# Performance work log

Measured on AMD Instinct MI355X. Metric: run time of the kernel, lower is better.

Reference implementation:

```python
import jax, jax.numpy as jnp
import numpy as np

B, L, D_MODEL, N_HEADS = 2, 2048, 1024, 16
D_HEAD = D_MODEL // N_HEADS
EPS = 1e-5


def setup_inputs() -> dict:
    key = jax.random.key(0)
    ks = jax.random.split(key, 10)
    x = jax.random.normal(ks[0], (B, L, D_MODEL), dtype=jnp.float32)
    # causal boolean mask [B, L, L]
    attn_mask = jnp.broadcast_to(jnp.tril(jnp.ones((L, L), dtype=bool)), (B, L, L))
    ts = jax.random.randint(ks[1], (B, L), 0, 10000)
    rope_lambda = jax.random.uniform(ks[2], (B, L, 1), dtype=jnp.float32)
    q_gate = jax.random.uniform(ks[3], (B, L, N_HEADS), dtype=jnp.float32)
    k_gate = jax.random.uniform(ks[4], (B, L, N_HEADS), dtype=jnp.float32)
    v_gate = jax.random.uniform(ks[5], (B, L, N_HEADS), dtype=jnp.float32)
    type_pair_bias = jax.random.normal(ks[6], (B, 1, L, L), dtype=jnp.float32)
    # parameters (torch Linear convention: y = x @ W.T + b)
    proj_w = jax.random.normal(ks[7], (4 * D_MODEL, D_MODEL), dtype=jnp.float32) * 0.02
    proj_b = jnp.zeros((4 * D_MODEL,), dtype=jnp.float32)
    out_w = jax.random.normal(ks[8], (D_MODEL, D_MODEL), dtype=jnp.float32) * 0.02
    out_b = jnp.zeros((D_MODEL,), dtype=jnp.float32)
    head_scale = jnp.ones((N_HEADS,), dtype=jnp.float32) * (D_HEAD ** -0.5)
    ln_gamma = jnp.ones((D_MODEL,), dtype=jnp.float32)
    ln_beta = jnp.zeros((D_MODEL,), dtype=jnp.float32)
    return {"x": x, "attn_mask": attn_mask, "ts": ts, "rope_lambda": rope_lambda,
            "q_gate": q_gate, "k_gate": k_gate, "v_gate": v_gate,
            "type_pair_bias": type_pair_bias, "proj_w": proj_w, "proj_b": proj_b,
            "out_w": out_w, "out_b": out_b, "head_scale": head_scale,
            "ln_gamma": ln_gamma, "ln_beta": ln_beta}


def _split_heads(t):
    b, l, _ = t.shape
    return t.reshape(b, l, N_HEADS, D_HEAD).transpose(0, 2, 1, 3)  # [B,H,L,Dh]


def _apply_rope(q, k, rope_lambda):
    # behavior-module RoPE: positions from cumsum of rope_lambda
    pos = jnp.cumsum(rope_lambda[..., 0], axis=1)  # [B, L]
    inv_freq = 1.0 / (10000.0 ** (jnp.arange(0, D_HEAD, 2, dtype=jnp.float32) / D_HEAD))
    freqs = pos[:, None, :, None] * inv_freq[None, None, None, :]  # [B,1,L,Dh/2]
    cos, sin = jnp.cos(freqs), jnp.sin(freqs)

    def rot(t):
        te, to = t[..., 0::2], t[..., 1::2]
        return jnp.concatenate([te * cos - to * sin, te * sin + to * cos], axis=-1)

    return rot(q), rot(k)


def reference(x, attn_mask, ts, rope_lambda, q_gate, k_gate, v_gate,
              type_pair_bias, proj_w, proj_b, out_w, out_b, head_scale,
              ln_gamma, ln_beta):
    b, l, d = x.shape
    h = jax.nn.silu(x @ proj_w.T + proj_b)  # [B,L,4D]
    u, v, q, k = jnp.split(h, 4, axis=-1)
    u, v, q, k = _split_heads(u), _split_heads(v), _split_heads(q), _split_heads(k)
    q, k = _apply_rope(q, k, rope_lambda)
    # multiplicative per-head gates: [B,L,H] -> [B,H,L,1]
    q = q * q_gate.transpose(0, 2, 1)[..., None]
    k = k * k_gate.transpose(0, 2, 1)[..., None]
    v = v * v_gate.transpose(0, 2, 1)[..., None]
    logits = jnp.einsum('bhid,bhjd->bhij', q, k)
    logits = logits * head_scale[None, :, None, None]
    # original does two adds: + type_pair_bias and + 3.0 * type_pair_bias
    logits = logits + type_pair_bias
    logits = logits + 3.0 * type_pair_bias
    logits = jax.nn.silu(logits)  # non-softmax SiLU attention
    logits = jnp.where(attn_mask[:, None, :, :], logits, 0.0)
    y = jnp.einsum('bhij,bhjd->bhid', logits, v)  # [B,H,L,Dh]
    y = y.transpose(0, 2, 1, 3).reshape(b, l, d)
    y = y * u.transpose(0, 2, 1, 3).reshape(b, l, d)  # gated output
    y = y @ out_w.T + out_b
    r = x + y  # dropout is identity in eval mode
    mu = jnp.mean(r, axis=-1, keepdims=True)
    var = jnp.mean((r - mu) ** 2, axis=-1, keepdims=True)
    return (r - mu) / jnp.sqrt(var + EPS) * ln_gamma + ln_beta
```

## Files before the change

### kernel.cpp

```cpp
#include <hip/hip_runtime.h>
#include <cstdint>
#include <cstddef>

typedef unsigned short u16;
typedef __attribute__((ext_vector_type(8))) short short8v;
typedef __attribute__((ext_vector_type(4))) float f32x4;

#define B_   2
#define L_   2048
#define D_   1024
#define NH_  16
#define DH_  64
#define M_   (B_*L_)
#define N4_  (4*D_)

__device__ __forceinline__ float bf2f(u16 u) {
  union { float f; unsigned int i; } v; v.i = ((unsigned int)u) << 16; return v.f;
}
__device__ __forceinline__ u16 f2bf(float f) {
  union { float f; unsigned int i; } v; v.f = f;
  unsigned int x = v.i;
  return (u16)((x + 0x7fffu + ((x >> 16) & 1u)) >> 16);
}
__device__ __forceinline__ unsigned int pk_bf16(float a, float b) {
#if __has_builtin(__builtin_amdgcn_cvt_pk_bf16_f32)
  auto r = __builtin_amdgcn_cvt_pk_bf16_f32(a, b);
  union { decltype(r) v; unsigned int u; } c; c.v = r; return c.u;
#else
  return (unsigned int)f2bf(a) | ((unsigned int)f2bf(b) << 16);
#endif
}
__device__ __forceinline__ float siluf(float x) { return x / (1.0f + __expf(-x)); }

__device__ __forceinline__ void gl2lds16(const u16* g, u16* l) {
  __builtin_amdgcn_global_load_lds(
      (const __attribute__((address_space(1))) unsigned int*)(const void*)g,
      (__attribute__((address_space(3))) unsigned int*)(void*)l,
      16, 0, 0);
}

__global__ __launch_bounds__(256) void k_conv_cum(const float* __restrict__ x,
                                                  const float* __restrict__ pw,
                                                  const float* __restrict__ ow,
                                                  const float* __restrict__ lam,
                                                  u16* __restrict__ xb,
                                                  u16* __restrict__ pwb,
                                                  u16* __restrict__ owb,
                                                  float* __restrict__ pos) {
  const int NX = M_ * D_ / 4, NP = N4_ * D_ / 4;
  int bid = blockIdx.x;
  int tid = threadIdx.x;
  if (bid < 9216) {
    int i = bid * 256 + tid;
    const float* src; u16* dst; int j;
    if (i < NX)            { src = x;  dst = xb;  j = i; }
    else if (i < NX + NP)  { src = pw; dst = pwb; j = i - NX; }
    else                   { src = ow; dst = owb; j = i - NX - NP; }
    float4 v = ((const float4*)src)[j];
    ushort4 o; o.x = f2bf(v.x); o.y = f2bf(v.y); o.z = f2bf(v.z); o.w = f2bf(v.w);
    ((ushort4*)dst)[j] = o;
  } else {
    int b = bid - 9216;
    const float* in = lam + (size_t)b * L_;
    float* out = pos + (size_t)b * L_;
    float loc[8], s = 0.0f;
#pragma unroll
    for (int i = 0; i < 8; ++i) { loc[i] = in[tid * 8 + i]; s += loc[i]; }
    __shared__ float sb[256];
    sb[tid] = s;
    __syncthreads();
    for (int off = 1; off < 256; off <<= 1) {
      float t = (tid >= off) ? sb[tid - off] : 0.0f;
      __syncthreads();
      sb[tid] += t;
      __syncthreads();
    }
    float run = sb[tid] - s;
#pragma unroll
    for (int i = 0; i < 8; ++i) { run += loc[i]; out[tid * 8 + i] = run; }
  }
}

__global__ __launch_bounds__(256, 4) void k_gemm1(const u16* __restrict__ A,
                                                  const u16* __restrict__ Bw,
                                                  const float* __restrict__ bias,
                                                  u16* __restrict__ hu, u16* __restrict__ hv,
                                                  u16* __restrict__ hq, u16* __restrict__ hk) {
  const int K = D_;
  int bn = blockIdx.x, bm = blockIdx.y, tid = threadIdx.x;
  int w = tid >> 6, lane = tid & 63, quad = lane >> 4, r16 = lane & 15;
  __shared__ __align__(16) u16 As[8192], Bs[8192];
  const u16* gA = A  + (size_t)(bm * 128) * K;
  const u16* gB = Bw + (size_t)(bn * 128) * K;
  int srow = tid >> 2, sc = tid & 3;
#pragma unroll
  for (int s = 0; s < 2; ++s) {
    int row = s * 64 + srow;
    int q = (sc - (row >> 1)) & 3;
    gl2lds16(gA + (size_t)row * K + q * 8, As + s * 2048 + w * 512);
    gl2lds16(gB + (size_t)row * K + q * 8, Bs + s * 2048 + w * 512);
  }
  f32x4 acc[4][4] = {};
  int wm = w & 1, wn = w >> 1;
  const int rowb = wm * 64, colb = wn * 64;
  for (int n = 0; n < 32; ++n) {
    __syncthreads();
    if (n + 1 < 32) {
      int kt = (n + 1) * 32, pb = (n + 1) & 1;
#pragma unroll
      for (int s = 0; s < 2; ++s) {
        int row = s * 64 + srow;
        int q = (sc - (row >> 1)) & 3;
        gl2lds16(gA + (size_t)row * K + kt + q * 8, As + pb * 4096 + s * 2048 + w * 512);
        gl2lds16(gB + (size_t)row * K + kt + q * 8, Bs + pb * 4096 + s * 2048 + w * 512);
      }
    }
    const u16* Ab = As + (n & 1) * 4096;
    const u16* Bb = Bs + (n & 1) * 4096;
    short8v af[4], bf[4];
#pragma unroll
    for (int mi = 0; mi < 4; ++mi) {
      int row = rowb + mi * 16 + r16;
      af[mi] = *(const short8v*)(Ab + (row * 4 + ((quad + (row >> 1)) & 3)) * 8);
    }
#pragma unroll
    for (int ni = 0; ni < 4; ++ni) {
      int row = colb + ni * 16 + r16;
      bf[ni] = *(const short8v*)(Bb + (row * 4 + ((quad + (row >> 1)) & 3)) * 8);
    }
#pragma unroll
    for (int mi = 0; mi < 4; ++mi)
#pragma unroll
      for (int ni = 0; ni < 4; ++ni)
        acc[mi][ni] = __builtin_amdgcn_mfma_f32_16x16x32_bf16(af[mi], bf[ni], acc[mi][ni], 0, 0, 0);
  }
  int nb = (bn * 128) >> 10;
  u16* dst = (nb == 0) ? hu : (nb == 1) ? hv : (nb == 2) ? hq : hk;
  int cbase = (bn * 128) & 1023;
  int row0 = bm * 128 + rowb;
#pragma unroll
  for (int ni = 0; ni < 4; ++ni) {
    int gcol = bn * 128 + colb + ni * 16 + r16;
    int lcol = cbase + colb + ni * 16 + r16;
    float bb = bias[gcol];
#pragma unroll
    for (int mi = 0; mi < 4; ++mi)
#pragma unroll
      for (int r = 0; r < 4; ++r) {
        int row = row0 + mi * 16 + quad * 4 + r;
        dst[(size_t)row * D_ + lcol] = f2bf(siluf(acc[mi][ni][r] + bb));
      }
  }
}

__global__ __launch_bounds__(256) void k_rope_vt(const u16* __restrict__ hq, const u16* __restrict__ hk,
                                                 const u16* __restrict__ hv,
                                                 const float* __restrict__ pos,
                                                 const float* __restrict__ qg, const float* __restrict__ kg,
                                                 const float* __restrict__ vg,
                                                 const float* __restrict__ hsc,
                                                 u16* __restrict__ Qb, u16* __restrict__ Kb,
                                                 u16* __restrict__ Vtb) {
  int bid = blockIdx.x;
  int tid = threadIdx.x;
  if (bid < 2048) {
    int idx = bid * 256 + tid;
    int j4 = idx & 7;
    int l  = (idx >> 3) & 2047;
    int bh = idx >> 14;
    int b = bh >> 4, hh = bh & 15;
    int row = b * L_ + l;
    float p = pos[row];
    float qs = qg[(size_t)row * NH_ + hh] * hsc[hh];
    float kgv = kg[(size_t)row * NH_ + hh];
    const u16* hqr = hq + (size_t)row * D_ + hh * DH_ + j4 * 8;
    const u16* hkr = hk + (size_t)row * D_ + hh * DH_ + j4 * 8;
    short8v qv = *(const short8v*)hqr;
    short8v kv = *(const short8v*)hkr;
    size_t ob = ((size_t)bh * L_ + l) * DH_ + j4 * 4;
    u16 qeo[4], qoo[4], keo[4], koo[4];
#pragma unroll
    for (int t = 0; t < 4; ++t) {
      int j = j4 * 4 + t;
      float inv = __expf(-(float)j * 0.28782313662425574f);
      float a = p * inv;
      float c, s;
      __sincosf(a, &s, &c);
      float qe = bf2f((u16)qv[2 * t]), qo = bf2f((u16)qv[2 * t + 1]);
      float ke = bf2f((u16)kv[2 * t]), ko = bf2f((u16)kv[2 * t + 1]);
      qeo[t] = f2bf((qe * c - qo * s) * qs);
      qoo[t] = f2bf((qe * s + qo * c) * qs);
      keo[t] = f2bf((ke * c - ko * s) * kgv);
      koo[t] = f2bf((ke * s + ko * c) * kgv);
    }
    *(ushort4*)(Qb + ob)      = make_ushort4(qeo[0], qeo[1], qeo[2], qeo[3]);
    *(ushort4*)(Qb + ob + 32) = make_ushort4(qoo[0], qoo[1], qoo[2], qoo[3]);
    *(ushort4*)(Kb + ob)      = make_ushort4(keo[0], keo[1], keo[2], keo[3]);
    *(ushort4*)(Kb + ob + 32) = make_ushort4(koo[0], koo[1], koo[2], koo[3]);
  } else {
    int b2 = bid - 2048;
    int lt = b2 & 31;
    int bh = b2 >> 5;
    int b = bh >> 4, hh = bh & 15;
    __shared__ u16 t[64][68];
    {
      int r = tid >> 2, cg = tid & 3;
      int row = b * L_ + lt * 64 + r;
      float gv = vg[(size_t)row * NH_ + hh];
      const u16* src = hv + (size_t)row * D_ + hh * DH_ + cg * 16;
      short8v v0 = ((const short8v*)src)[0];
      short8v v1 = ((const short8v*)src)[1];
#pragma unroll
      for (int e = 0; e < 8; ++e) {
        t[r][cg * 16 + e]     = f2bf(bf2f((u16)v0[e]) * gv);
        t[r][cg * 16 + 8 + e] = f2bf(bf2f((u16)v1[e]) * gv);
      }
    }
    __syncthreads();
    {
      int d = tid >> 2, lg = tid & 3;
      short8v o0, o1;
#pragma unroll
      for (int e = 0; e < 8; ++e) o0[e] = (short)t[lg * 16 + e][d];
#pragma unroll
      for (int e = 0; e < 8; ++e) o1[e] = (short)t[lg * 16 + 8 + e][d];
      u16* dst = Vtb + ((size_t)bh * DH_ + d) * L_ + lt * 64 + lg * 16;
      ((short8v*)dst)[0] = o0;
      ((short8v*)dst)[1] = o1;
    }
  }
}

__global__ __launch_bounds__(256, 3) void k_attn(const u16* __restrict__ Qb, const u16* __restrict__ Kb,
                                                 const u16* __restrict__ Vtb, const float* __restrict__ tpb,
                                                 const u16* __restrict__ hu, u16* __restrict__ A2) {
  int id = blockIdx.x;
  int group = id >> 5, bh = id & 31;
  int i64 = (group & 1) ? (group >> 1) : (31 - (group >> 1));
  int jmax = i64 >> 1;
  int b = bh >> 4, hh = bh & 15;
  int tid = threadIdx.x, w = tid >> 6, lane = tid & 63, quad = lane >> 4, r16 = lane & 15;
  int wj = w & 1, wi = w >> 1;
  __shared__ __align__(16) u16 Ks[8192];
  __shared__ __align__(16) u16 Vs[8192];
  __shared__ __align__(16) u16 Ps[8704];
  const size_t bhbase = (size_t)bh * L_ * DH_;
  int gibase = i64 * 64 + wi * 32;
  const u16* qt = Qb + bhbase + (size_t)gibase * DH_;
  short8v bq[2][2];
#pragma unroll
  for (int ks = 0; ks < 2; ++ks)
#pragma unroll
    for (int ti = 0; ti < 2; ++ti)
      bq[ks][ti] = *(const short8v*)(qt + (size_t)(ti * 16 + r16) * DH_ + ks * 32 + quad * 8);
#pragma unroll
  for (int s = 0; s < 4; ++s) {
    int row = (s & 1) * 64 + (tid >> 2);
    int q = ((tid & 3) - (row >> 1)) & 3;
    gl2lds16(Kb + bhbase + (size_t)row * DH_ + (s >> 1) * 32 + q * 8, Ks + s * 2048 + w * 512);
  }
  const float* bpr[2];
#pragma unroll
  for (int ti = 0; ti < 2; ++ti)
    bpr[ti] = tpb + ((size_t)b * L_ + gibase + ti * 16 + r16) * L_ + wj * 64 + quad * 4;
  float4 bv[4][2];
#pragma unroll
  for (int tj = 0; tj < 4; ++tj)
#pragma unroll
    for (int ti = 0; ti < 2; ++ti)
      if (tj * 16 + wj * 64 <= gibase + ti * 16 + 15)
        bv[tj][ti] = *(const float4*)(bpr[ti] + tj * 16);
  f32x4 accy[4] = {};
  int gimax_w = i64 * 64 + w * 16 + 15;
  for (int jt = 0; jt <= jmax; ++jt) {
    __syncthreads();
#pragma unroll
    for (int s = 0; s < 4; ++s) {
      int row = tid >> 2;
      int q = ((tid & 3) - (row >> 1)) & 3;
      gl2lds16(Vtb + bhbase + (size_t)row * L_ + jt * 128 + s * 32 + q * 8, Vs + s * 2048 + w * 512);
    }
#pragma unroll
    for (int tj = 0; tj < 4; ++tj) {
      int jlo = jt * 128 + wj * 64 + tj * 16;
      bool anyM = jlo <= gibase + 31;
      short8v ak0, ak1;
      if (anyM) {
        int row = wj * 64 + tj * 16 + r16;
        int sw = (quad + (row >> 1)) & 3;
        ak0 = *(const short8v*)(Ks + (row * 4 + sw) * 8);
        ak1 = *(const short8v*)(Ks + 4096 + (row * 4 + sw) * 8);
      }
#pragma unroll
      for (int ti = 0; ti < 2; ++ti) {
        int gmaxt = gibase + ti * 16 + 15;
        bool doM = jlo <= gmaxt;
        bool doW = (jlo & ~31) <= gmaxt;
        if (!doW) continue;
        unsigned int p01 = 0, p23 = 0;
        if (doM) {
          int gi = gibase + ti * 16 + r16;
          f32x4 acc = {};
          acc = __builtin_amdgcn_mfma_f32_16x16x32_bf16(ak0, bq[0][ti], acc, 0, 0, 0);
          acc = __builtin_amdgcn_mfma_f32_16x16x32_bf16(ak1, bq[1][ti], acc, 0, 0, 0);
          int j0 = jlo + quad * 4;
          float4 bvv = bv[tj][ti];
          float v0 = (j0     <= gi) ? siluf(fmaf(4.0f, bvv.x, acc[0])) : 0.0f;
          float v1 = (j0 + 1 <= gi) ? siluf(fmaf(4.0f, bvv.y, acc[1])) : 0.0f;
          float v2 = (j0 + 2 <= gi) ? siluf(fmaf(4.0f, bvv.z, acc[2])) : 0.0f;
          float v3 = (j0 + 3 <= gi) ? siluf(fmaf(4.0f, bvv.w, acc[3])) : 0.0f;
          p01 = pk_bf16(v0, v1);
          p23 = pk_bf16(v2, v3);
        }
        int iloc = wi * 32 + ti * 16 + r16;
        int rot = ((iloc >> 3) & 1) << 3;
        int col = wj * 64 + tj * 16 + quad * 4;
        *(uint2*)(Ps + iloc * 136 + (col & 96) + (((col & 31) + rot) & 31)) = make_uint2(p01, p23);
      }
    }
    __syncthreads();
    if (jt < jmax) {
      const size_t kb = bhbase + (size_t)(jt + 1) * 128 * DH_;
#pragma unroll
      for (int s = 0; s < 4; ++s) {
        int row = (s & 1) * 64 + (tid >> 2);
        int q = ((tid & 3) - (row >> 1)) & 3;
        gl2lds16(Kb + kb + (size_t)row * DH_ + (s >> 1) * 32 + q * 8, Ks + s * 2048 + w * 512);
      }
      int jn = (jt + 1) * 128;
#pragma unroll
      for (int tj = 0; tj < 4; ++tj)
#pragma unroll
        for (int ti = 0; ti < 2; ++ti)
          if (jn + tj * 16 + wj * 64 <= gibase + ti * 16 + 15)
            bv[tj][ti] = *(const float4*)(bpr[ti] + jn + tj * 16);
    }
#pragma unroll
    for (int ks = 0; ks < 4; ++ks) {
      if (jt * 128 + ks * 32 > gimax_w) continue;
      int li = w * 16 + r16;
      int rotr = ((li >> 3) & 1) << 3;
      short8v pa = *(const short8v*)(Ps + li * 136 + ks * 32 + ((quad * 8 + rotr) & 31));
#pragma unroll
      for (int ni = 0; ni < 4; ++ni) {
        int row = ni * 16 + r16;
        short8v vb = *(const short8v*)(Vs + ks * 2048 + (row * 4 + ((quad + (row >> 1)) & 3)) * 8);
        accy[ni] = __builtin_amdgcn_mfma_f32_16x16x32_bf16(pa, vb, accy[ni], 0, 0, 0);
      }
    }
  }
#pragma unroll
  for (int ni = 0; ni < 4; ++ni) {
    int d = ni * 16 + r16;
#pragma unroll
    for (int r = 0; r < 4; ++r) {
      int lr = w * 16 + quad * 4 + r;
      size_t rowg = (size_t)b * L_ + (size_t)i64 * 64 + lr;
      float u = bf2f(hu[rowg * D_ + hh * DH_ + d]);
      A2[rowg * D_ + hh * DH_ + d] = f2bf(accy[ni][r] * u);
    }
  }
}

__global__ __launch_bounds__(256, 4) void k_gemm2(const u16* __restrict__ A,
                                                  const u16* __restrict__ Bw,
                                                  const float* __restrict__ bias,
                                                  const float* __restrict__ xres,
                                                  float* __restrict__ out) {
  const int K = D_;
  int bn = blockIdx.x, bm = blockIdx.y, tid = threadIdx.x;
  int w = tid >> 6, lane = tid & 63, quad = lane >> 4, r16 = lane & 15;
  __shared__ __align__(16) u16 As[8192], Bs[8192];
  const u16* gA = A  + (size_t)(bm * 128) * K;
  const u16* gB = Bw + (size_t)(bn * 128) * K;
  int srow = tid >> 2, sc = tid & 3;
#pragma unroll
  for (int s = 0; s < 2; ++s) {
    int row = s * 64 + srow;
    int q = (sc - (row >> 1)) & 3;
    gl2lds16(gA + (size_t)row * K + q * 8, As + s * 2048 + w * 512);
    gl2lds16(gB + (size_t)row * K + q * 8, Bs + s * 2048 + w * 512);
  }
  f32x4 acc[4][4] = {};
  int wm = w & 1, wn = w >> 1;
  const int rowb = wm * 64, colb = wn * 64;
  for (int n = 0; n < 32; ++n) {
    __syncthreads();
    if (n + 1 < 32) {
      int kt = (n + 1) * 32, pb = (n + 1) & 1;
#pragma unroll
      for (int s = 0; s < 2; ++s) {
        int row = s * 64 + srow;
        int q = (sc - (row >> 1)) & 3;
        gl2lds16(gA + (size_t)row * K + kt + q * 8, As + pb * 4096 + s * 2048 + w * 512);
        gl2lds16(gB + (size_t)row * K + kt + q * 8, Bs + pb * 4096 + s * 2048 + w * 512);
      }
    }
    const u16* Ab = As + (n & 1) * 4096;
    const u16* Bb = Bs + (n & 1) * 4096;
    short8v af[4], bf[4];
#pragma unroll
    for (int mi = 0; mi < 4; ++mi) {
      int row = rowb + mi * 16 + r16;
      af[mi] = *(const short8v*)(Ab + (row * 4 + ((quad + (row >> 1)) & 3)) * 8);
    }
#pragma unroll
    for (int ni = 0; ni < 4; ++ni) {
      int row = colb + ni * 16 + r16;
      bf[ni] = *(const short8v*)(Bb + (row * 4 + ((quad + (row >> 1)) & 3)) * 8);
    }
#pragma unroll
    for (int mi = 0; mi < 4; ++mi)
#pragma unroll
      for (int ni = 0; ni < 4; ++ni)
        acc[mi][ni] = __builtin_amdgcn_mfma_f32_16x16x32_bf16(af[mi], bf[ni], acc[mi][ni], 0, 0, 0);
  }
  int row0 = bm * 128 + rowb, col0 = bn * 128 + colb;
#pragma unroll
  for (int ni = 0; ni < 4; ++ni) {
    int col = col0 + ni * 16 + r16;
    float bb = bias[col];
#pragma unroll
    for (int mi = 0; mi < 4; ++mi)
#pragma unroll
      for (int r = 0; r < 4; ++r) {
        int row = row0 + mi * 16 + quad * 4 + r;
        out[(size_t)row * D_ + col] = acc[mi][ni][r] + bb + xres[(size_t)row * D_ + col];
      }
  }
}

__global__ __launch_bounds__(256) void k_ln(float* __restrict__ r,
                                            const float* __restrict__ g,
                                            const float* __restrict__ be) {
  int row = blockIdx.x, tid = threadIdx.x;
  float* pr = r + (size_t)row * D_;
  __shared__ float s1[4], s2[4];
  float v[4];
#pragma unroll
  for (int i = 0; i < 4; ++i) v[i] = pr[i * 256 + tid];
  float s = v[0] + v[1] + v[2] + v[3];
#pragma unroll
  for (int o = 32; o > 0; o >>= 1) s += __shfl_down(s, o, 64);
  if ((tid & 63) == 0) s1[tid >> 6] = s;
  __syncthreads();
  float mu = (s1[0] + s1[1] + s1[2] + s1[3]) * (1.0f / D_);
  float d = 0.0f;
#pragma unroll
  for (int i = 0; i < 4; ++i) { float t = v[i] - mu; d += t * t; }
#pragma unroll
  for (int o = 32; o > 0; o >>= 1) d += __shfl_down(d, o, 64);
  if ((tid & 63) == 0) s2[tid >> 6] = d;
  __syncthreads();
  float var = (s2[0] + s2[1] + s2[2] + s2[3]) * (1.0f / D_);
  float inv = rsqrtf(var + 1e-5f);
#pragma unroll
  for (int i = 0; i < 4; ++i) {
    int c = i * 256 + tid;
    pr[c] = (v[i] - mu) * inv * g[c] + be[c];
  }
}

extern "C" void kernel_launch(void* const* d_in, const int* in_sizes, int n_in,
                              void* d_out, int out_size, void* d_ws, size_t ws_size,
                              hipStream_t stream) {
  const float* x   = (const float*)d_in[0];
  const float* lam = (const float*)d_in[3];
  const float* qg  = (const float*)d_in[4];
  const float* kg  = (const float*)d_in[5];
  const float* vg  = (const float*)d_in[6];
  const float* tpb = (const float*)d_in[7];
  const float* pw  = (const float*)d_in[8];
  const float* pb  = (const float*)d_in[9];
  const float* ow  = (const float*)d_in[10];
  const float* ob  = (const float*)d_in[11];
  const float* hsc = (const float*)d_in[12];
  const float* lng = (const float*)d_in[13];
  const float* lnb = (const float*)d_in[14];
  float* out = (float*)d_out;

  char* ws = (char*)d_ws;
  u16* xb   = (u16*)(ws + 0);
  u16* pwb  = (u16*)(ws + 8388608);
  u16* owb  = (u16*)(ws + 16777216);
  u16* hu   = (u16*)(ws + 18874368);
  u16* hv   = (u16*)(ws + 27262976);
  u16* hq   = (u16*)(ws + 35651584);
  u16* hk   = (u16*)(ws + 44040192);
  float* pos = (float*)(ws + 52428800);
  u16* Qb  = xb;
  u16* Kb  = pwb;
  u16* Vtb = hq;
  u16* A2  = hk;

  k_conv_cum<<<9218, 256, 0, stream>>>(x, pw, ow, lam, xb, pwb, owb, pos);
  k_gemm1<<<dim3(32, 32), 256, 0, stream>>>(xb, pwb, pb, hu, hv, hq, hk);
  k_rope_vt<<<3072, 256, 0, stream>>>(hq, hk, hv, pos, qg, kg, vg, hsc, Qb, Kb, Vtb);
  k_attn<<<1024, 256, 0, stream>>>(Qb, Kb, Vtb, tpb, hu, A2);
  k_gemm2<<<dim3(8, 32), 256, 0, stream>>>(A2, owb, ob, x, out);
  k_ln<<<4096, 256, 0, stream>>>(out, lng, lnb);
}
```

Measured before the change: 314.9 us.

## Keep attention probabilities in registers via permlane swaps instead of LDS staging

Each wave now owns a full 16-row strip of queries across all 128 key columns, so the QK^T output it produces is exactly what it needs as the A operand of the PV MFMA. The 16x16 C-layout fragments are rearranged into the 16x32 A-operand layout with v_permlane32/16_swap instead of being written to and read back from a shared P buffer. This removes the Ps LDS buffer and its traffic, which allows raising the occupancy hint to 4 blocks. SiLU now uses a fast reciprocal, and the packed bf16 fallback uses inline asm. The cost is more registers per wave, which may work against the higher occupancy target, and the K tile is no longer shared across two waves in the i dimension.

```diff
diff --git a/kernel.cpp b/kernel.cpp
--- a/kernel.cpp
+++ b/kernel.cpp
@@ -27,10 +27,14 @@
   auto r = __builtin_amdgcn_cvt_pk_bf16_f32(a, b);
   union { decltype(r) v; unsigned int u; } c; c.v = r; return c.u;
 #else
-  return (unsigned int)f2bf(a) | ((unsigned int)f2bf(b) << 16);
+  unsigned int r;
+  asm("v_cvt_pk_bf16_f32 %0, %1, %2" : "=v"(r) : "v"(a), "v"(b));
+  return r;
 #endif
 }
-__device__ __forceinline__ float siluf(float x) { return x / (1.0f + __expf(-x)); }
+__device__ __forceinline__ float siluf(float x) {
+  return x * __builtin_amdgcn_rcpf(1.0f + __expf(-x));
+}
 
 __device__ __forceinline__ void gl2lds16(const u16* g, u16* l) {
   __builtin_amdgcn_global_load_lds(
@@ -231,7 +235,7 @@
   }
 }
 
-__global__ __launch_bounds__(256, 3) void k_attn(const u16* __restrict__ Qb, const u16* __restrict__ Kb,
+__global__ __launch_bounds__(256, 4) void k_attn(const u16* __restrict__ Qb, const u16* __restrict__ Kb,
                                                  const u16* __restrict__ Vtb, const float* __restrict__ tpb,
                                                  const u16* __restrict__ hu, u16* __restrict__ A2) {
   int id = blockIdx.x;
@@ -240,38 +244,28 @@
   int jmax = i64 >> 1;
   int b = bh >> 4, hh = bh & 15;
   int tid = threadIdx.x, w = tid >> 6, lane = tid & 63, quad = lane >> 4, r16 = lane & 15;
-  int wj = w & 1, wi = w >> 1;
   __shared__ __align__(16) u16 Ks[8192];
   __shared__ __align__(16) u16 Vs[8192];
-  __shared__ __align__(16) u16 Ps[8704];
   const size_t bhbase = (size_t)bh * L_ * DH_;
-  int gibase = i64 * 64 + wi * 32;
-  const u16* qt = Qb + bhbase + (size_t)gibase * DH_;
-  short8v bq[2][2];
+  int irow = i64 * 64 + w * 16;
+  int gimax_w = irow + 15;
+  const u16* qt = Qb + bhbase + (size_t)irow * DH_;
+  short8v bq[2];
 #pragma unroll
   for (int ks = 0; ks < 2; ++ks)
-#pragma unroll
-    for (int ti = 0; ti < 2; ++ti)
-      bq[ks][ti] = *(const short8v*)(qt + (size_t)(ti * 16 + r16) * DH_ + ks * 32 + quad * 8);
+    bq[ks] = *(const short8v*)(qt + (size_t)r16 * DH_ + ks * 32 + quad * 8);
 #pragma unroll
   for (int s = 0; s < 4; ++s) {
     int row = (s & 1) * 64 + (tid >> 2);
     int q = ((tid & 3) - (row >> 1)) & 3;
     gl2lds16(Kb + bhbase + (size_t)row * DH_ + (s >> 1) * 32 + q * 8, Ks + s * 2048 + w * 512);
   }
-  const float* bpr[2];
-#pragma unroll
-  for (int ti = 0; ti < 2; ++ti)
-    bpr[ti] = tpb + ((size_t)b * L_ + gibase + ti * 16 + r16) * L_ + wj * 64 + quad * 4;
-  float4 bv[4][2];
-#pragma unroll
-  for (int tj = 0; tj < 4; ++tj)
-#pragma unroll
-    for (int ti = 0; ti < 2; ++ti)
-      if (tj * 16 + wj * 64 <= gibase + ti * 16 + 15)
-        bv[tj][ti] = *(const float4*)(bpr[ti] + tj * 16);
+  const float* bpr = tpb + ((size_t)b * L_ + irow + r16) * L_ + quad * 4;
+  float4 bv[8];
+#pragma unroll
+  for (int tj = 0; tj < 8; ++tj)
+    if (tj * 16 <= gimax_w) bv[tj] = *(const float4*)(bpr + tj * 16);
   f32x4 accy[4] = {};
-  int gimax_w = i64 * 64 + w * 16 + 15;
   for (int jt = 0; jt <= jmax; ++jt) {
     __syncthreads();
 #pragma unroll
@@ -280,31 +274,27 @@
       int q = ((tid & 3) - (row >> 1)) & 3;
       gl2lds16(Vtb + bhbase + (size_t)row * L_ + jt * 128 + s * 32 + q * 8, Vs + s * 2048 + w * 512);
     }
-#pragma unroll
-    for (int tj = 0; tj < 4; ++tj) {
-      int jlo = jt * 128 + wj * 64 + tj * 16;
-      bool anyM = jlo <= gibase + 31;
-      short8v ak0, ak1;
-      if (anyM) {
-        int row = wj * 64 + tj * 16 + r16;
-        int sw = (quad + (row >> 1)) & 3;
-        ak0 = *(const short8v*)(Ks + (row * 4 + sw) * 8);
-        ak1 = *(const short8v*)(Ks + 4096 + (row * 4 + sw) * 8);
-      }
-#pragma unroll
-      for (int ti = 0; ti < 2; ++ti) {
-        int gmaxt = gibase + ti * 16 + 15;
-        bool doM = jlo <= gmaxt;
-        bool doW = (jlo & ~31) <= gmaxt;
-        if (!doW) continue;
+    unsigned int paw[4][4];
+#pragma unroll
+    for (int ks2 = 0; ks2 < 4; ++ks2) {
+      if (jt * 128 + ks2 * 32 > gimax_w) continue;
+      unsigned int W[2][2];
+#pragma unroll
+      for (int t = 0; t < 2; ++t) {
+        int tj = 2 * ks2 + t;
+        int jlo = jt * 128 + tj * 16;
         unsigned int p01 = 0, p23 = 0;
-        if (doM) {
-          int gi = gibase + ti * 16 + r16;
+        if (jlo <= gimax_w) {
+          int row = tj * 16 + r16;
+          int sw = (quad + (row >> 1)) & 3;
+          short8v ak0 = *(const short8v*)(Ks + (row * 4 + sw) * 8);
+          short8v ak1 = *(const short8v*)(Ks + 4096 + (row * 4 + sw) * 8);
           f32x4 acc = {};
-          acc = __builtin_amdgcn_mfma_f32_16x16x32_bf16(ak0, bq[0][ti], acc, 0, 0, 0);
-          acc = __builtin_amdgcn_mfma_f32_16x16x32_bf16(ak1, bq[1][ti], acc, 0, 0, 0);
+          acc = __builtin_amdgcn_mfma_f32_16x16x32_bf16(ak0, bq[0], acc, 0, 0, 0);
+          acc = __builtin_amdgcn_mfma_f32_16x16x32_bf16(ak1, bq[1], acc, 0, 0, 0);
+          int gi = irow + r16;
           int j0 = jlo + quad * 4;
-          float4 bvv = bv[tj][ti];
+          float4 bvv = bv[tj];
           float v0 = (j0     <= gi) ? siluf(fmaf(4.0f, bvv.x, acc[0])) : 0.0f;
           float v1 = (j0 + 1 <= gi) ? siluf(fmaf(4.0f, bvv.y, acc[1])) : 0.0f;
           float v2 = (j0 + 2 <= gi) ? siluf(fmaf(4.0f, bvv.z, acc[2])) : 0.0f;
@@ -312,10 +302,15 @@
           p01 = pk_bf16(v0, v1);
           p23 = pk_bf16(v2, v3);
         }
-        int iloc = wi * 32 + ti * 16 + r16;
-        int rot = ((iloc >> 3) & 1) << 3;
-        int col = wj * 64 + tj * 16 + quad * 4;
-        *(uint2*)(Ps + iloc * 136 + (col & 96) + (((col & 31) + rot) & 31)) = make_uint2(p01, p23);
+        W[t][0] = p01; W[t][1] = p23;
+      }
+#pragma unroll
+      for (int p = 0; p < 2; ++p) {
+        unsigned int x = W[0][p], y = W[1][p];
+        asm("v_permlane32_swap_b32 %0, %1" : "+v"(x), "+v"(y));
+        asm("v_permlane16_swap_b32 %0, %1" : "+v"(x), "+v"(y));
+        paw[ks2][p]     = x;
+        paw[ks2][2 + p] = y;
       }
     }
     __syncthreads();
@@ -329,18 +324,15 @@
       }
       int jn = (jt + 1) * 128;
 #pragma unroll
-      for (int tj = 0; tj < 4; ++tj)
-#pragma unroll
-        for (int ti = 0; ti < 2; ++ti)
-          if (jn + tj * 16 + wj * 64 <= gibase + ti * 16 + 15)
-            bv[tj][ti] = *(const float4*)(bpr[ti] + jn + tj * 16);
+      for (int tj = 0; tj < 8; ++tj)
+        if (jn + tj * 16 <= gimax_w) bv[tj] = *(const float4*)(bpr + jn + tj * 16);
     }
 #pragma unroll
     for (int ks = 0; ks < 4; ++ks) {
       if (jt * 128 + ks * 32 > gimax_w) continue;
-      int li = w * 16 + r16;
-      int rotr = ((li >> 3) & 1) << 3;
-      short8v pa = *(const short8v*)(Ps + li * 136 + ks * 32 + ((quad * 8 + rotr) & 31));
+      union { unsigned int u[4]; short8v s; } pu;
+      pu.u[0] = paw[ks][0]; pu.u[1] = paw[ks][1]; pu.u[2] = paw[ks][2]; pu.u[3] = paw[ks][3];
+      short8v pa = pu.s;
 #pragma unroll
       for (int ni = 0; ni < 4; ++ni) {
         int row = ni * 16 + r16;
```

Measured after the change: 313.2 us. Within noise of the previous version (-0.6%).
